# Kernel optimization log

Measured on AMD Instinct MI355X. Metric: run time of the kernel, lower is better.

The kernel has to match this reference:

```python
import jax, jax.numpy as jnp
import numpy as np

B, S, D = 256, 1024, 32   # batch, seq_len, raw feature dim
H, L = 128, 2             # hidden_dim, num_layers
IN = D + 2                # GRU input: features + mask + time-delta


def setup_inputs() -> dict:
    key = jax.random.key(0)
    ks = jax.random.split(key, 16)
    x = jax.random.normal(ks[0], (B, S, D), jnp.float32)
    nan_mask = jax.random.bernoulli(ks[1], 0.3, (B, S))
    x = jnp.where(nan_mask[:, :, None], jnp.nan, x)  # missing timesteps are all-NaN
    # strictly increasing timestamps shared across batch
    t = jnp.cumsum(jax.random.uniform(ks[2], (S,), jnp.float32, 0.1, 1.0))

    def init(k, shape):
        s = 1.0 / np.sqrt(H)
        return jax.random.uniform(k, shape, jnp.float32, -s, s)

    params = {}
    in_dims = [IN, H]
    for l in range(L):
        params[f"Wih{l}"] = init(ks[3 + 4 * l], (3 * H, in_dims[l]))
        params[f"Whh{l}"] = init(ks[4 + 4 * l], (3 * H, H))
        params[f"bih{l}"] = init(ks[5 + 4 * l], (3 * H,))
        params[f"bhh{l}"] = init(ks[6 + 4 * l], (3 * H,))
    return {"t": t, "x": x, **params}


def _impute(t, x):
    # mask[b,i] = 1 if timestep i of sample b is missing (any NaN feature)
    mask = jnp.isnan(x).any(-1)                      # [B,S] bool
    # prev[b,i] = last observed index strictly before i, or -1 (parallel cummax)
    idx = jnp.where(~mask, jnp.arange(S)[None, :], -1)
    cmax = jax.lax.cummax(idx, axis=1)
    prev = jnp.concatenate([jnp.full((B, 1), -1), cmax[:, :-1]], axis=1)  # [B,S]
    prev_c = jnp.clip(prev, 0, S - 1)
    x_clean = jnp.nan_to_num(x)
    x_prev = jnp.take_along_axis(x_clean, prev_c[:, :, None], axis=1)
    # masked: forward-fill from last observation (zeros if none); unmasked: keep x
    imputed = jnp.where(mask[:, :, None],
                        jnp.where((prev >= 0)[:, :, None], x_prev, 0.0),
                        x_clean)
    # time delta: t[i]-t[prev] when a previous observation exists, else raw t delta
    t_deltas = jnp.concatenate([jnp.zeros((1,), t.dtype), t[1:] - t[:-1]])
    t_exp = jnp.where(prev >= 0, t[None, :] - t[prev_c], t_deltas[None, :])  # [B,S]
    return jnp.concatenate([imputed,
                            mask.astype(jnp.float32)[:, :, None],
                            t_exp[:, :, None]], axis=-1)  # [B,S,D+2]


def _gru_layer(xseq, Wih, Whh, bih, bhh):
    # precompute input projections for all timesteps (one big GEMM)
    gx = jnp.einsum('bsd,gd->bsg', xseq, Wih) + bih  # [B,S,3H], gate order r,z,n

    def step(h, g):
        gh = h @ Whh.T + bhh
        r = jax.nn.sigmoid(g[:, :H] + gh[:, :H])
        z = jax.nn.sigmoid(g[:, H:2 * H] + gh[:, H:2 * H])
        n = jnp.tanh(g[:, 2 * H:] + r * gh[:, 2 * H:])
        h = (1.0 - z) * n + z * h
        return h, h

    h0 = jnp.zeros((xseq.shape[0], H), xseq.dtype)
    _, hs = jax.lax.scan(step, h0, gx.transpose(1, 0, 2))
    return hs.transpose(1, 0, 2)  # [B,S,H]


def reference(t, x, Wih0, Whh0, bih0, bhh0, Wih1, Whh1, bih1, bhh1):
    inp = _impute(t, x)
    h = _gru_layer(inp, Wih0, Whh0, bih0, bhh0)
    h = _gru_layer(h, Wih1, Whh1, bih1, bhh1)
    return h[:, -1, :]  # [B,H]
```

## Files before the change

### kernel.cpp

```cpp
#include <hip/hip_runtime.h>
#include <hip/hip_bf16.h>


#define BB 256
#define SS 1024
#define DD 32
#define HH 128
#define NT 768

typedef _Float16 f16;
typedef __attribute__((ext_vector_type(2))) _Float16 h2;
typedef __attribute__((ext_vector_type(16))) int i32x16;
typedef __attribute__((ext_vector_type(8))) int i32x8;

__device__ inline h2 as_h2(int x) { union { int i; h2 h; } u; u.i = x; return u.h; }

__device__ inline float dot2(h2 a, h2 b, float c) {
    return __builtin_amdgcn_fdot2(a, b, c, false);
}

__device__ inline const void* uniform_ptr(const void* p) {
    unsigned long long u = (unsigned long long)p;
    unsigned lo = __builtin_amdgcn_readfirstlane((unsigned)u);
    unsigned hi = __builtin_amdgcn_readfirstlane((unsigned)(u >> 32));
    return (const void*)(((unsigned long long)hi << 32) | (unsigned long long)lo);
}

template<int OFF>
__device__ inline i32x16 sload_x16(const void* p) {
    i32x16 r;
    asm volatile("s_load_dwordx16 %0, %1, %2" : "=s"(r) : "s"(p), "i"(OFF));
    return r;
}
template<int OFF>
__device__ inline i32x8 sload_x8(const void* p) {
    i32x8 r;
    asm volatile("s_load_dwordx8 %0, %1, %2" : "=s"(r) : "s"(p), "i"(OFF));
    return r;
}
template<int OFF>
__device__ inline int sload_x1(const void* p) {
    int r;
    asm volatile("s_load_dword %0, %1, %2" : "=s"(r) : "s"(p), "i"(OFF));
    return r;
}

__device__ inline float frcp(float x) { return __builtin_amdgcn_rcpf(x); }
__device__ inline float fast_sigm(float x) { return frcp(1.0f + __expf(-x)); }
__device__ inline float fast_tanh(float x) {
    x = fminf(15.0f, fmaxf(-15.0f, x));
    float e = __expf(-2.0f * x);
    return (1.0f - e) * frcp(1.0f + e);
}

struct ImpState { float xprev, tprev; bool hasprev; };

__device__ inline void impute_store(int i, float xv, int l, ImpState& st,
                                    f16* hxg, const float* tb) {
    bool nanp = (l < 32) && (xv != xv);
    unsigned long long bal = __ballot(nanp);
    bool mask = bal != 0ull;
    if (l < 32) {
        float imp = mask ? st.xprev : xv;
        hxg[l] = (f16)imp;
        if (!mask) st.xprev = xv;
    }
    float tcur = tb[i];
    float tdel = (i == 0) ? 0.0f : (tcur - tb[i - 1]);
    float texp = st.hasprev ? (tcur - st.tprev) : tdel;
    if (l == 32) hxg[32] = (f16)(mask ? 1.0f : 0.0f);
    if (l == 33) hxg[33] = (f16)texp;
    if (!mask) { st.hasprev = true; st.tprev = tcur; }
}

__global__ __launch_bounds__(NT, 3) void gru_fused(
    const float* __restrict__ t_in, const float* __restrict__ x_in,
    const float* __restrict__ Wih0, const float* __restrict__ Whh0,
    const float* __restrict__ bih0, const float* __restrict__ bhh0,
    const float* __restrict__ Wih1, const float* __restrict__ Whh1,
    const float* __restrict__ bih1, const float* __restrict__ bhh1,
    float* __restrict__ out, char* __restrict__ ws)
{
    __shared__ float tb[SS];
    __shared__ float4 pcomb[NT];

    const int tid = threadIdx.x;
    const int b = blockIdx.x;
    const int group = tid >= 384;
    const int row = tid - 384 * group;

    char* base = ws + (size_t)b * 1024;
    char* h0p = base;
    char* h1p = base + 256;
    char* hxp = base + 512;

    h2 wih0[9], whh0[32], wih1[32], whh1[32];
    {
        const float* p = Wih0 + row * 34;
        const int lim = 8 + group;
        #pragma unroll
        for (int k = 0; k < 9; k++) {
            int e = 16 * group + 2 * k;
            f16 lo = (k < lim) ? (f16)p[e]     : (f16)0.0f;
            f16 hi = (k < lim) ? (f16)p[e + 1] : (f16)0.0f;
            h2 v = {lo, hi}; wih0[k] = v;
        }
        p = Whh0 + row * HH + 64 * group;
        #pragma unroll
        for (int k = 0; k < 32; k++) { h2 v = {(f16)p[2*k], (f16)p[2*k+1]}; whh0[k] = v; }
        p = Wih1 + row * HH + 64 * group;
        #pragma unroll
        for (int k = 0; k < 32; k++) { h2 v = {(f16)p[2*k], (f16)p[2*k+1]}; wih1[k] = v; }
        p = Whh1 + row * HH + 64 * group;
        #pragma unroll
        for (int k = 0; k < 32; k++) { h2 v = {(f16)p[2*k], (f16)p[2*k+1]}; whh1[k] = v; }
    }

    const bool isU = (tid >= 512);
    const bool isU0 = (tid >= 512 && tid < 640);
    const int j = isU0 ? (tid - 512) : (tid - 640);
    float ubi[3], ubh[3]; float hr = 0.0f;
    if (isU) {
        const float* bi = isU0 ? bih0 : bih1;
        const float* bh = isU0 ? bhh0 : bhh1;
        #pragma unroll
        for (int q = 0; q < 3; q++) { ubi[q] = bi[j + 128*q]; ubh[q] = bh[j + 128*q]; }
    }

    for (int i2 = tid; i2 < SS; i2 += NT) tb[i2] = t_in[i2];
    if (tid < 64)        ((int*)h0p)[tid]       = 0;
    else if (tid < 128)  ((int*)h1p)[tid - 64]  = 0;
    else if (tid < 146)  ((int*)hxp)[tid - 128] = 0;

    const float* xrow = x_in + (size_t)b * SS * DD + tid;
    ImpState st; st.xprev = 0.0f; st.tprev = 0.0f; st.hasprev = false;

    __syncthreads();
    if (tid < 64) {
        float xv0 = (tid < 32) ? xrow[0] : 0.0f;
        impute_store(0, xv0, tid, st, (f16*)hxp, tb);
    }
    __syncthreads();

    const void* h0g  = uniform_ptr(h0p + 128 * group);
    const void* h1g  = uniform_ptr(h1p + 128 * group);
    const void* hxg8 = uniform_ptr(hxp + 32 * group);
    const void* hxg1 = uniform_ptr(hxp + (group ? 64 : 32));

    for (int i = 0; i <= SS; ++i) {
        const bool doL0 = (i < SS), doL1 = (i > 0), doImp = (i + 1 < SS);

        asm volatile("s_dcache_inv" ::: "memory");
        i32x16 h0a = sload_x16<0>(h0g);
        i32x16 h0b = sload_x16<64>(h0g);
        i32x16 h1a = sload_x16<0>(h1g);
        i32x16 h1b = sload_x16<64>(h1g);
        i32x8  hxv = sload_x8<0>(hxg8);
        int    hxe = sload_x1<0>(hxg1);

        float xv_n = 0.0f;
        if (tid < 32 && doImp) xv_n = xrow[(size_t)(i + 1) * DD];

        asm volatile("s_waitcnt lgkmcnt(0)"
                     : "+s"(h0a), "+s"(h0b), "+s"(h1a), "+s"(h1b), "+s"(hxv), "+s"(hxe)
                     :: "memory");

        float aP = 0.0f;
        #pragma unroll
        for (int k = 0; k < 9; k++) {
            int d = (k < 8) ? hxv[k] : hxe;
            aP = dot2(as_h2(d), wih0[k], aP);
        }
        float cC[4] = {0,0,0,0}, dC[4] = {0,0,0,0}, eC[4] = {0,0,0,0};
        #pragma unroll
        for (int k = 0; k < 32; k++) {
            h2 hh = as_h2((k < 16) ? h0a[k] : h0b[k - 16]);
            cC[k & 3] = dot2(hh, whh0[k], cC[k & 3]);
            dC[k & 3] = dot2(hh, wih1[k], dC[k & 3]);
        }
        #pragma unroll
        for (int k = 0; k < 32; k++) {
            h2 hh = as_h2((k < 16) ? h1a[k] : h1b[k - 16]);
            eC[k & 3] = dot2(hh, whh1[k], eC[k & 3]);
        }
        float cP = (cC[0] + cC[1]) + (cC[2] + cC[3]);
        float dP = (dC[0] + dC[1]) + (dC[2] + dC[3]);
        float eP = (eC[0] + eC[1]) + (eC[2] + eC[3]);
        pcomb[tid] = make_float4(aP, cP, dP, eP);
        __syncthreads();

        if (isU) {
            bool act = isU0 ? doL0 : doL1;
            if (act) {
                float4 pa0 = pcomb[j],       pb0 = pcomb[384 + j];
                float4 pa1 = pcomb[j + 128], pb1 = pcomb[384 + j + 128];
                float4 pa2 = pcomb[j + 256], pb2 = pcomb[384 + j + 256];
                float rx, rh, zx, zh, nx, nh;
                if (isU0) {
                    rx = pa0.x + pb0.x; rh = pa0.y + pb0.y;
                    zx = pa1.x + pb1.x; zh = pa1.y + pb1.y;
                    nx = pa2.x + pb2.x; nh = pa2.y + pb2.y;
                } else {
                    rx = pa0.z + pb0.z; rh = pa0.w + pb0.w;
                    zx = pa1.z + pb1.z; zh = pa1.w + pb1.w;
                    nx = pa2.z + pb2.z; nh = pa2.w + pb2.w;
                }
                float r = fast_sigm(ubi[0] + ubh[0] + rx + rh);
                float z = fast_sigm(ubi[1] + ubh[1] + zx + zh);
                float n = fast_tanh(ubi[2] + nx + r * (ubh[2] + nh));
                hr = (1.0f - z) * n + z * hr;
                f16* hp = (f16*)(isU0 ? h0p : h1p);
                hp[j] = (f16)hr;
            }
        } else if (tid < 64 && doImp) {
            impute_store(i + 1, xv_n, tid, st, (f16*)hxp, tb);
        }
        __syncthreads();
    }

    if (tid >= 640) out[(size_t)b * HH + (tid - 640)] = hr;
}

extern "C" void kernel_launch(void* const* d_in, const int* in_sizes, int n_in,
                              void* d_out, int out_size, void* d_ws, size_t ws_size,
                              hipStream_t stream) {
    gru_fused<<<dim3(BB), dim3(NT), 0, stream>>>(
        (const float*)d_in[0], (const float*)d_in[1],
        (const float*)d_in[2], (const float*)d_in[3],
        (const float*)d_in[4], (const float*)d_in[5],
        (const float*)d_in[6], (const float*)d_in[7],
        (const float*)d_in[8], (const float*)d_in[9],
        (float*)d_out, (char*)d_ws);
}
```

Before: 1.365 ms.

## Keep GRU hidden state in LDS and broadcast via readlane instead of scalar loads

The per-step hidden state and imputed input move from a global workspace, read through scalar loads after a scalar-cache invalidate, into shared memory. Each wave reads one dword per lane from LDS and broadcasts the values to scalars with readlane. The partial-sum buffer also changes from one float4 array to four separate float arrays. This is meant to cut the latency of the cache invalidate and the round trip through global memory on every one of the 1025 serial steps, at the cost of about 73 readlane instructions per step.

```diff
diff --git a/kernel.cpp b/kernel.cpp
--- a/kernel.cpp
+++ b/kernel.cpp
@@ -10,39 +10,11 @@
 
 typedef _Float16 f16;
 typedef __attribute__((ext_vector_type(2))) _Float16 h2;
-typedef __attribute__((ext_vector_type(16))) int i32x16;
-typedef __attribute__((ext_vector_type(8))) int i32x8;
 
 __device__ inline h2 as_h2(int x) { union { int i; h2 h; } u; u.i = x; return u.h; }
 
 __device__ inline float dot2(h2 a, h2 b, float c) {
     return __builtin_amdgcn_fdot2(a, b, c, false);
-}
-
-__device__ inline const void* uniform_ptr(const void* p) {
-    unsigned long long u = (unsigned long long)p;
-    unsigned lo = __builtin_amdgcn_readfirstlane((unsigned)u);
-    unsigned hi = __builtin_amdgcn_readfirstlane((unsigned)(u >> 32));
-    return (const void*)(((unsigned long long)hi << 32) | (unsigned long long)lo);
-}
-
-template<int OFF>
-__device__ inline i32x16 sload_x16(const void* p) {
-    i32x16 r;
-    asm volatile("s_load_dwordx16 %0, %1, %2" : "=s"(r) : "s"(p), "i"(OFF));
-    return r;
-}
-template<int OFF>
-__device__ inline i32x8 sload_x8(const void* p) {
-    i32x8 r;
-    asm volatile("s_load_dwordx8 %0, %1, %2" : "=s"(r) : "s"(p), "i"(OFF));
-    return r;
-}
-template<int OFF>
-__device__ inline int sload_x1(const void* p) {
-    int r;
-    asm volatile("s_load_dword %0, %1, %2" : "=s"(r) : "s"(p), "i"(OFF));
-    return r;
 }
 
 __device__ inline float frcp(float x) { return __builtin_amdgcn_rcpf(x); }
@@ -56,20 +28,20 @@
 struct ImpState { float xprev, tprev; bool hasprev; };
 
 __device__ inline void impute_store(int i, float xv, int l, ImpState& st,
-                                    f16* hxg, const float* tb) {
+                                    f16* hxf, const float* tb) {
     bool nanp = (l < 32) && (xv != xv);
     unsigned long long bal = __ballot(nanp);
     bool mask = bal != 0ull;
     if (l < 32) {
         float imp = mask ? st.xprev : xv;
-        hxg[l] = (f16)imp;
+        hxf[l] = (f16)imp;
         if (!mask) st.xprev = xv;
     }
     float tcur = tb[i];
     float tdel = (i == 0) ? 0.0f : (tcur - tb[i - 1]);
     float texp = st.hasprev ? (tcur - st.tprev) : tdel;
-    if (l == 32) hxg[32] = (f16)(mask ? 1.0f : 0.0f);
-    if (l == 33) hxg[33] = (f16)texp;
+    if (l == 32) hxf[32] = (f16)(mask ? 1.0f : 0.0f);
+    if (l == 33) hxf[33] = (f16)texp;
     if (!mask) { st.hasprev = true; st.tprev = tcur; }
 }
 
@@ -79,20 +51,17 @@
     const float* __restrict__ bih0, const float* __restrict__ bhh0,
     const float* __restrict__ Wih1, const float* __restrict__ Whh1,
     const float* __restrict__ bih1, const float* __restrict__ bhh1,
-    float* __restrict__ out, char* __restrict__ ws)
+    float* __restrict__ out)
 {
     __shared__ float tb[SS];
-    __shared__ float4 pcomb[NT];
+    __shared__ int stDW[152];
+    __shared__ float pA[NT], pC[NT], pD[NT], pE[NT];
 
     const int tid = threadIdx.x;
     const int b = blockIdx.x;
     const int group = tid >= 384;
     const int row = tid - 384 * group;
-
-    char* base = ws + (size_t)b * 1024;
-    char* h0p = base;
-    char* h1p = base + 256;
-    char* hxp = base + 512;
+    const int lane = tid & 63;
 
     h2 wih0[9], whh0[32], wih1[32], whh1[32];
     {
@@ -127,10 +96,16 @@
         for (int q = 0; q < 3; q++) { ubi[q] = bi[j + 128*q]; ubh[q] = bh[j + 128*q]; }
     }
 
+    const int idxA = (lane < 32) ? (32 * group + lane)
+                                 : (64 + 32 * group + (lane - 32));
+    const int idxB = 128 + 8 * group + ((lane < 9) ? lane : 0);
+
     for (int i2 = tid; i2 < SS; i2 += NT) tb[i2] = t_in[i2];
-    if (tid < 64)        ((int*)h0p)[tid]       = 0;
-    else if (tid < 128)  ((int*)h1p)[tid - 64]  = 0;
-    else if (tid < 146)  ((int*)hxp)[tid - 128] = 0;
+    if (tid < 152) stDW[tid] = 0;
+
+    f16* h0f = (f16*)&stDW[0];
+    f16* h1f = (f16*)&stDW[64];
+    f16* hxf = (f16*)&stDW[128];
 
     const float* xrow = x_in + (size_t)b * SS * DD + tid;
     ImpState st; st.xprev = 0.0f; st.tprev = 0.0f; st.hasprev = false;
@@ -138,82 +113,69 @@
     __syncthreads();
     if (tid < 64) {
         float xv0 = (tid < 32) ? xrow[0] : 0.0f;
-        impute_store(0, xv0, tid, st, (f16*)hxp, tb);
+        impute_store(0, xv0, tid, st, hxf, tb);
     }
     __syncthreads();
-
-    const void* h0g  = uniform_ptr(h0p + 128 * group);
-    const void* h1g  = uniform_ptr(h1p + 128 * group);
-    const void* hxg8 = uniform_ptr(hxp + 32 * group);
-    const void* hxg1 = uniform_ptr(hxp + (group ? 64 : 32));
 
     for (int i = 0; i <= SS; ++i) {
         const bool doL0 = (i < SS), doL1 = (i > 0), doImp = (i + 1 < SS);
 
-        asm volatile("s_dcache_inv" ::: "memory");
-        i32x16 h0a = sload_x16<0>(h0g);
-        i32x16 h0b = sload_x16<64>(h0g);
-        i32x16 h1a = sload_x16<0>(h1g);
-        i32x16 h1b = sload_x16<64>(h1g);
-        i32x8  hxv = sload_x8<0>(hxg8);
-        int    hxe = sload_x1<0>(hxg1);
+        int vA = stDW[idxA];
+        int vB = stDW[idxB];
 
         float xv_n = 0.0f;
         if (tid < 32 && doImp) xv_n = xrow[(size_t)(i + 1) * DD];
 
-        asm volatile("s_waitcnt lgkmcnt(0)"
-                     : "+s"(h0a), "+s"(h0b), "+s"(h1a), "+s"(h1b), "+s"(hxv), "+s"(hxe)
-                     :: "memory");
+        int h0u[32], h1u[32], hxu[9];
+        #pragma unroll
+        for (int k = 0; k < 32; k++) h0u[k] = __builtin_amdgcn_readlane(vA, k);
+        #pragma unroll
+        for (int k = 0; k < 32; k++) h1u[k] = __builtin_amdgcn_readlane(vA, 32 + k);
+        #pragma unroll
+        for (int k = 0; k < 9; k++)  hxu[k] = __builtin_amdgcn_readlane(vB, k);
 
         float aP = 0.0f;
         #pragma unroll
-        for (int k = 0; k < 9; k++) {
-            int d = (k < 8) ? hxv[k] : hxe;
-            aP = dot2(as_h2(d), wih0[k], aP);
-        }
+        for (int k = 0; k < 9; k++) aP = dot2(as_h2(hxu[k]), wih0[k], aP);
         float cC[4] = {0,0,0,0}, dC[4] = {0,0,0,0}, eC[4] = {0,0,0,0};
         #pragma unroll
         for (int k = 0; k < 32; k++) {
-            h2 hh = as_h2((k < 16) ? h0a[k] : h0b[k - 16]);
+            h2 hh = as_h2(h0u[k]);
             cC[k & 3] = dot2(hh, whh0[k], cC[k & 3]);
             dC[k & 3] = dot2(hh, wih1[k], dC[k & 3]);
         }
         #pragma unroll
         for (int k = 0; k < 32; k++) {
-            h2 hh = as_h2((k < 16) ? h1a[k] : h1b[k - 16]);
+            h2 hh = as_h2(h1u[k]);
             eC[k & 3] = dot2(hh, whh1[k], eC[k & 3]);
         }
-        float cP = (cC[0] + cC[1]) + (cC[2] + cC[3]);
-        float dP = (dC[0] + dC[1]) + (dC[2] + dC[3]);
-        float eP = (eC[0] + eC[1]) + (eC[2] + eC[3]);
-        pcomb[tid] = make_float4(aP, cP, dP, eP);
+        pA[tid] = aP;
+        pC[tid] = (cC[0] + cC[1]) + (cC[2] + cC[3]);
+        pD[tid] = (dC[0] + dC[1]) + (dC[2] + dC[3]);
+        pE[tid] = (eC[0] + eC[1]) + (eC[2] + eC[3]);
         __syncthreads();
 
         if (isU) {
             bool act = isU0 ? doL0 : doL1;
             if (act) {
-                float4 pa0 = pcomb[j],       pb0 = pcomb[384 + j];
-                float4 pa1 = pcomb[j + 128], pb1 = pcomb[384 + j + 128];
-                float4 pa2 = pcomb[j + 256], pb2 = pcomb[384 + j + 256];
                 float rx, rh, zx, zh, nx, nh;
                 if (isU0) {
-                    rx = pa0.x + pb0.x; rh = pa0.y + pb0.y;
-                    zx = pa1.x + pb1.x; zh = pa1.y + pb1.y;
-                    nx = pa2.x + pb2.x; nh = pa2.y + pb2.y;
+                    rx = pA[j]       + pA[384 + j];       rh = pC[j]       + pC[384 + j];
+                    zx = pA[j + 128] + pA[384 + j + 128]; zh = pC[j + 128] + pC[384 + j + 128];
+                    nx = pA[j + 256] + pA[384 + j + 256]; nh = pC[j + 256] + pC[384 + j + 256];
                 } else {
-                    rx = pa0.z + pb0.z; rh = pa0.w + pb0.w;
-                    zx = pa1.z + pb1.z; zh = pa1.w + pb1.w;
-                    nx = pa2.z + pb2.z; nh = pa2.w + pb2.w;
+                    rx = pD[j]       + pD[384 + j];       rh = pE[j]       + pE[384 + j];
+                    zx = pD[j + 128] + pD[384 + j + 128]; zh = pE[j + 128] + pE[384 + j + 128];
+                    nx = pD[j + 256] + pD[384 + j + 256]; nh = pE[j + 256] + pE[384 + j + 256];
                 }
                 float r = fast_sigm(ubi[0] + ubh[0] + rx + rh);
                 float z = fast_sigm(ubi[1] + ubh[1] + zx + zh);
                 float n = fast_tanh(ubi[2] + nx + r * (ubh[2] + nh));
                 hr = (1.0f - z) * n + z * hr;
-                f16* hp = (f16*)(isU0 ? h0p : h1p);
-                hp[j] = (f16)hr;
+                (isU0 ? h0f : h1f)[j] = (f16)hr;
             }
         } else if (tid < 64 && doImp) {
-            impute_store(i + 1, xv_n, tid, st, (f16*)hxp, tb);
+            impute_store(i + 1, xv_n, tid, st, hxf, tb);
         }
         __syncthreads();
     }
@@ -230,5 +192,5 @@
         (const float*)d_in[4], (const float*)d_in[5],
         (const float*)d_in[6], (const float*)d_in[7],
         (const float*)d_in[8], (const float*)d_in[9],
-        (float*)d_out, (char*)d_ws);
+        (float*)d_out);
 }
```

New measurement: 1.570 ms. +15.0%, slower.
